# Kernel tuning notes

Hardware: AMD Instinct MI355X
Metric: run time of the kernel (lower is better)

## Reference

```python
import jax, jax.numpy as jnp
import numpy as np

N = 50000
IN_CH = 512
OUT_CH = 512
DEG = 32
E = N * DEG


def setup_inputs() -> dict:
    key = jax.random.key(0)
    kx, kwc, kwn, kb, ke = jax.random.split(key, 5)
    x = jax.random.normal(kx, (N, IN_CH), dtype=jnp.float32)
    bound = 1.0 / np.sqrt(IN_CH)
    wc = jax.random.uniform(kwc, (IN_CH, OUT_CH), minval=-bound, maxval=bound, dtype=jnp.float32)
    wn = jax.random.uniform(kwn, (IN_CH, OUT_CH), minval=-bound, maxval=bound, dtype=jnp.float32)
    bias = jax.random.uniform(kb, (OUT_CH,), minval=-bound, maxval=bound, dtype=jnp.float32)
    # Every node appears as a source exactly DEG times -> no empty-neighborhood NaNs.
    src = jnp.repeat(jnp.arange(N, dtype=jnp.int64), DEG)
    dst = jax.random.randint(ke, (E,), 0, N, dtype=jnp.int64)
    edge_index = jnp.stack([src, dst], axis=0)  # [2, E]
    return {"x": x, "wc": wc, "wn": wn, "bias": bias, "edge_index": edge_index}


def reference(x, wc, wn, bias, edge_index):
    # alpha = x @ wc ; beta = x @ wn
    alpha = x @ wc                       # [N, out]
    beta = x @ wn                        # [N, out]
    src, dst = edge_index[0], edge_index[1]
    # gamma[n] = mean_{e: src[e]==n} beta[dst[e]]
    sums = jax.ops.segment_sum(beta[dst], src, num_segments=x.shape[0])          # [N, out]
    counts = jax.ops.segment_sum(jnp.ones_like(src, dtype=beta.dtype), src,
                                 num_segments=x.shape[0])                        # [N]
    gamma = sums / counts[:, None]
    return alpha + gamma + bias
```

## Files before the change

### kernel.cpp

```cpp
#include <hip/hip_runtime.h>


#define M_ROWS 50000
#define DEG 32
#define NE (M_ROWS * DEG)

typedef short s16x8 __attribute__((ext_vector_type(8)));
typedef float f32x4 __attribute__((ext_vector_type(4)));
typedef float f32x2 __attribute__((ext_vector_type(2)));

__device__ __forceinline__ unsigned short f2bf(float f) {
  union { float f; unsigned int u; } c; c.f = f;
  unsigned int u = c.u;
  u += 0x7fffu + ((u >> 16) & 1u);
  return (unsigned short)(u >> 16);
}

__device__ __forceinline__ unsigned char f2fp8(float f) {
  int p = __builtin_amdgcn_cvt_pk_fp8_f32(f, f, 0, false);
  return (unsigned char)(p & 0xff);
}

__device__ __forceinline__ float bfhi(unsigned int u) {
  return __uint_as_float(u & 0xffff0000u);
}
__device__ __forceinline__ float bflo(unsigned int u) {
  return __uint_as_float(u << 16);
}

__device__ __forceinline__ void gl_lds16(const void* g, void* l) {
  __builtin_amdgcn_global_load_lds(
      (const __attribute__((address_space(1))) unsigned int*)g,
      (__attribute__((address_space(3))) unsigned int*)l, 16, 0, 0);
}

__global__ __launch_bounds__(256) void k_convert_x(
    const float* __restrict__ x, unsigned short* __restrict__ xb) {
  const size_t base = ((size_t)blockIdx.x * 256 + threadIdx.x) * 8;
  const float4 a = *(const float4*)(x + base);
  const float4 b = *(const float4*)(x + base + 4);
  union { unsigned short u[8]; uint4 v; } p;
  p.u[0] = f2bf(a.x); p.u[1] = f2bf(a.y); p.u[2] = f2bf(a.z); p.u[3] = f2bf(a.w);
  p.u[4] = f2bf(b.x); p.u[5] = f2bf(b.y); p.u[6] = f2bf(b.z); p.u[7] = f2bf(b.w);
  *(uint4*)(xb + base) = p.v;
}

__global__ __launch_bounds__(256) void k_convert_w(
    const float* __restrict__ wc, const float* __restrict__ wn,
    unsigned short* __restrict__ wt) {
  const int k = blockIdx.x;
  const int n4 = threadIdx.x * 4;
  const float* src = (n4 < 512) ? (wc + (size_t)k * 512 + n4)
                                : (wn + (size_t)k * 512 + (n4 - 512));
  const float4 v = *(const float4*)src;
  wt[(size_t)(n4 + 0) * 512 + k] = f2bf(v.x);
  wt[(size_t)(n4 + 1) * 512 + k] = f2bf(v.y);
  wt[(size_t)(n4 + 2) * 512 + k] = f2bf(v.z);
  wt[(size_t)(n4 + 3) * 512 + k] = f2bf(v.w);
}

__global__ __launch_bounds__(256) void k_gemm(
    const unsigned short* __restrict__ xb,
    const unsigned short* __restrict__ wt,
    const float* __restrict__ bias,
    unsigned short* __restrict__ alphab,
    unsigned char* __restrict__ betaf8) {
  __shared__ __attribute__((aligned(16))) unsigned short As[128 * 32];
  __shared__ __attribute__((aligned(16))) unsigned short Bs[128 * 32];

  const int tid = threadIdx.x;
  const int n0 = blockIdx.x * 128;
  const int m0 = blockIdx.y * 128;
  const int wv = tid >> 6;
  const int l = tid & 63;
  const int lm = l & 15;
  const int quad = l >> 4;
  const int mb = (wv >> 1) * 64;
  const int nb = (wv & 1) * 64;

  f32x4 acc[4][4];
#pragma unroll
  for (int i = 0; i < 4; ++i)
#pragma unroll
    for (int j = 0; j < 4; ++j) acc[i][j] = (f32x4)(0.0f);

  for (int kt = 0; kt < 16; ++kt) {
    const int k0 = kt * 32;
    __syncthreads();
#pragma unroll
    for (int s = 0; s < 2; ++s) {
      const int c = s * 256 + tid;
      const int row = c >> 2;
      const int seg = c & 3;
      int am = m0 + row; if (am >= M_ROWS) am = M_ROWS - 1;
      gl_lds16(xb + (size_t)am * 512 + (k0 + seg * 8),
               (char*)As + (size_t)(s * 256 + (tid & ~63)) * 16);
      gl_lds16(wt + (size_t)(n0 + row) * 512 + (k0 + seg * 8),
               (char*)Bs + (size_t)(s * 256 + (tid & ~63)) * 16);
    }
    __syncthreads();

    s16x8 af[4], bfr[4];
#pragma unroll
    for (int i = 0; i < 4; ++i)
      af[i] = *(const s16x8*)&As[(mb + 16 * i + lm) * 32 + quad * 8];
#pragma unroll
    for (int j = 0; j < 4; ++j)
      bfr[j] = *(const s16x8*)&Bs[(nb + 16 * j + lm) * 32 + quad * 8];
#pragma unroll
    for (int i = 0; i < 4; ++i)
#pragma unroll
      for (int j = 0; j < 4; ++j)
        acc[i][j] = __builtin_amdgcn_mfma_f32_16x16x32_bf16(
            af[i], bfr[j], acc[i][j], 0, 0, 0);
  }

  const bool isAlpha = (n0 < 512);
#pragma unroll
  for (int i = 0; i < 4; ++i) {
#pragma unroll
    for (int j = 0; j < 4; ++j) {
#pragma unroll
      for (int r = 0; r < 4; ++r) {
        const int m = m0 + mb + 16 * i + quad * 4 + r;
        if (m < M_ROWS) {
          const int n = n0 + nb + 16 * j + lm;
          const float v = acc[i][j][r];
          if (isAlpha) {
            alphab[(size_t)m * 512 + n] = f2bf(v + bias[n]);
          } else {
            betaf8[(size_t)m * 512 + (n - 512)] = f2fp8(v);
          }
        }
      }
    }
  }
}

__global__ __launch_bounds__(256) void k_gather(
    const int* __restrict__ dst, const uint2* __restrict__ beta8,
    const unsigned short* __restrict__ alphab, float* __restrict__ out) {
  const int node = blockIdx.x * 4 + (threadIdx.x >> 6);
  const int l = threadIdx.x & 63;
  const int idx = dst[(size_t)node * 32 + (l & 31)];
  f32x2 a01 = (f32x2)(0.0f), a23 = (f32x2)(0.0f),
        a45 = (f32x2)(0.0f), a67 = (f32x2)(0.0f);
#pragma unroll
  for (int j = 0; j < 32; ++j) {
    const int d = __builtin_amdgcn_readlane(idx, j);
    const uint2 b = beta8[(size_t)d * 64 + l];
    a01 += __builtin_amdgcn_cvt_pk_f32_fp8(b.x, false);
    a23 += __builtin_amdgcn_cvt_pk_f32_fp8(b.x, true);
    a45 += __builtin_amdgcn_cvt_pk_f32_fp8(b.y, false);
    a67 += __builtin_amdgcn_cvt_pk_f32_fp8(b.y, true);
  }
  const uint4 av = *(const uint4*)(alphab + (size_t)node * 512 + l * 8);
  const float s = 1.0f / 32.0f;
  float4 o0, o1;
  o0.x = bflo(av.x) + a01.x * s;
  o0.y = bfhi(av.x) + a01.y * s;
  o0.z = bflo(av.y) + a23.x * s;
  o0.w = bfhi(av.y) + a23.y * s;
  o1.x = bflo(av.z) + a45.x * s;
  o1.y = bfhi(av.z) + a45.y * s;
  o1.z = bflo(av.w) + a67.x * s;
  o1.w = bfhi(av.w) + a67.y * s;
  float4* o = (float4*)(out + (size_t)node * 512 + l * 8);
  o[0] = o0; o[1] = o1;
}

extern "C" void kernel_launch(void* const* d_in, const int* in_sizes, int n_in,
                              void* d_out, int out_size, void* d_ws, size_t ws_size,
                              hipStream_t stream) {
  const float* x    = (const float*)d_in[0];
  const float* wc   = (const float*)d_in[1];
  const float* wn   = (const float*)d_in[2];
  const float* bias = (const float*)d_in[3];
  const int*   ei   = (const int*)d_in[4];
  float* out = (float*)d_out;

  char* ws = (char*)d_ws;
  unsigned short* xb     = (unsigned short*)ws;
  unsigned short* wt     = (unsigned short*)(ws + 51200000);
  unsigned short* alphab = (unsigned short*)(ws + 52248576);
  unsigned char*  betaf8 = (unsigned char*)(ws + 103448576);

  k_convert_x<<<12500, 256, 0, stream>>>(x, xb);
  k_convert_w<<<512, 256, 0, stream>>>(wc, wn, wt);
  k_gemm<<<dim3(8, 391), 256, 0, stream>>>(xb, wt, bias, alphab, betaf8);
  k_gather<<<12500, 256, 0, stream>>>(ei + NE, (const uint2*)betaf8, alphab, out);
}
```

Baseline: 422.9 us.

## Widen GEMM K-tile with LDS swizzle, group tiles, and column-phase the gather

The GEMM now stages 64-wide K slices with an XOR-swizzled LDS layout to avoid bank conflicts. It precomputes load offsets, remaps blocks into groups of 8 M-tiles for better L2 reuse of activations, and hoists the bias loads. The gather is split into 8 column phases via a second grid dimension, so each phase touches only a 64-byte slice of every beta row. That keeps the randomly accessed working set small enough to stay L2-resident, with edges spread over lane groups and combined by cross-lane shuffles. The trade-off is narrower 4-byte gather loads, 8x more gather blocks, and only a quarter of the lanes doing the final stores.

```diff
diff --git a/kernel.cpp b/kernel.cpp
--- a/kernel.cpp
+++ b/kernel.cpp
@@ -65,12 +65,22 @@
     const float* __restrict__ bias,
     unsigned short* __restrict__ alphab,
     unsigned char* __restrict__ betaf8) {
-  __shared__ __attribute__((aligned(16))) unsigned short As[128 * 32];
-  __shared__ __attribute__((aligned(16))) unsigned short Bs[128 * 32];
+  __shared__ __attribute__((aligned(16))) unsigned short As[128 * 64];
+  __shared__ __attribute__((aligned(16))) unsigned short Bs[128 * 64];
 
   const int tid = threadIdx.x;
-  const int n0 = blockIdx.x * 128;
-  const int m0 = blockIdx.y * 128;
+  const int g = blockIdx.x;
+  int mt, nt;
+  if (g < 3072) {
+    const int c = g & 7, j = g >> 3;
+    nt = j & 7; mt = (j >> 3) * 8 + c;
+  } else {
+    const int r = g - 3072;
+    mt = 384 + (r >> 3); nt = r & 7;
+  }
+  const int n0 = nt * 128;
+  const int m0 = mt * 128;
+
   const int wv = tid >> 6;
   const int l = tid & 63;
   const int lm = l & 15;
@@ -78,44 +88,64 @@
   const int mb = (wv >> 1) * 64;
   const int nb = (wv & 1) * 64;
 
+  size_t aofs[4], bofs[4];
+  int ldst[4];
+#pragma unroll
+  for (int s = 0; s < 4; ++s) {
+    const int c = s * 256 + tid;
+    const int row = c >> 3;
+    const int seg = c & 7;
+    const int sg = seg ^ (row & 7);
+    int am = m0 + row; if (am >= M_ROWS) am = M_ROWS - 1;
+    aofs[s] = (size_t)am * 512 + sg * 8;
+    bofs[s] = (size_t)(n0 + row) * 512 + sg * 8;
+    ldst[s] = (s * 256 + (tid & ~63)) * 16;
+  }
+
   f32x4 acc[4][4];
 #pragma unroll
   for (int i = 0; i < 4; ++i)
 #pragma unroll
     for (int j = 0; j < 4; ++j) acc[i][j] = (f32x4)(0.0f);
 
-  for (int kt = 0; kt < 16; ++kt) {
-    const int k0 = kt * 32;
+  for (int kt = 0; kt < 8; ++kt) {
+    const int k0 = kt * 64;
     __syncthreads();
 #pragma unroll
-    for (int s = 0; s < 2; ++s) {
-      const int c = s * 256 + tid;
-      const int row = c >> 2;
-      const int seg = c & 3;
-      int am = m0 + row; if (am >= M_ROWS) am = M_ROWS - 1;
-      gl_lds16(xb + (size_t)am * 512 + (k0 + seg * 8),
-               (char*)As + (size_t)(s * 256 + (tid & ~63)) * 16);
-      gl_lds16(wt + (size_t)(n0 + row) * 512 + (k0 + seg * 8),
-               (char*)Bs + (size_t)(s * 256 + (tid & ~63)) * 16);
+    for (int s = 0; s < 4; ++s) {
+      gl_lds16(xb + aofs[s] + k0, (char*)As + ldst[s]);
+      gl_lds16(wt + bofs[s] + k0, (char*)Bs + ldst[s]);
     }
     __syncthreads();
 
-    s16x8 af[4], bfr[4];
-#pragma unroll
-    for (int i = 0; i < 4; ++i)
-      af[i] = *(const s16x8*)&As[(mb + 16 * i + lm) * 32 + quad * 8];
-#pragma unroll
-    for (int j = 0; j < 4; ++j)
-      bfr[j] = *(const s16x8*)&Bs[(nb + 16 * j + lm) * 32 + quad * 8];
-#pragma unroll
-    for (int i = 0; i < 4; ++i)
-#pragma unroll
-      for (int j = 0; j < 4; ++j)
-        acc[i][j] = __builtin_amdgcn_mfma_f32_16x16x32_bf16(
-            af[i], bfr[j], acc[i][j], 0, 0, 0);
+#pragma unroll
+    for (int h = 0; h < 2; ++h) {
+      s16x8 af[4], bfr[4];
+#pragma unroll
+      for (int i = 0; i < 4; ++i) {
+        const int R = mb + 16 * i + lm;
+        af[i] = *(const s16x8*)&As[R * 64 + (((h * 4 + quad) ^ (R & 7)) << 3)];
+      }
+#pragma unroll
+      for (int j = 0; j < 4; ++j) {
+        const int R = nb + 16 * j + lm;
+        bfr[j] = *(const s16x8*)&Bs[R * 64 + (((h * 4 + quad) ^ (R & 7)) << 3)];
+      }
+#pragma unroll
+      for (int i = 0; i < 4; ++i)
+#pragma unroll
+        for (int j = 0; j < 4; ++j)
+          acc[i][j] = __builtin_amdgcn_mfma_f32_16x16x32_bf16(
+              af[i], bfr[j], acc[i][j], 0, 0, 0);
+    }
   }
 
   const bool isAlpha = (n0 < 512);
+  float b4[4];
+#pragma unroll
+  for (int j = 0; j < 4; ++j)
+    b4[j] = isAlpha ? bias[n0 + nb + 16 * j + lm] : 0.0f;
+
 #pragma unroll
   for (int i = 0; i < 4; ++i) {
 #pragma unroll
@@ -127,7 +157,7 @@
           const int n = n0 + nb + 16 * j + lm;
           const float v = acc[i][j][r];
           if (isAlpha) {
-            alphab[(size_t)m * 512 + n] = f2bf(v + bias[n]);
+            alphab[(size_t)m * 512 + n] = f2bf(v + b4[j]);
           } else {
             betaf8[(size_t)m * 512 + (n - 512)] = f2fp8(v);
           }
@@ -138,35 +168,42 @@
 }
 
 __global__ __launch_bounds__(256) void k_gather(
-    const int* __restrict__ dst, const uint2* __restrict__ beta8,
+    const int* __restrict__ dst, const unsigned int* __restrict__ beta8,
     const unsigned short* __restrict__ alphab, float* __restrict__ out) {
+  const int phase = blockIdx.y;
   const int node = blockIdx.x * 4 + (threadIdx.x >> 6);
   const int l = threadIdx.x & 63;
+  const int grp = l >> 4;
+  const int lm = l & 15;
   const int idx = dst[(size_t)node * 32 + (l & 31)];
-  f32x2 a01 = (f32x2)(0.0f), a23 = (f32x2)(0.0f),
-        a45 = (f32x2)(0.0f), a67 = (f32x2)(0.0f);
-#pragma unroll
-  for (int j = 0; j < 32; ++j) {
-    const int d = __builtin_amdgcn_readlane(idx, j);
-    const uint2 b = beta8[(size_t)d * 64 + l];
-    a01 += __builtin_amdgcn_cvt_pk_f32_fp8(b.x, false);
-    a23 += __builtin_amdgcn_cvt_pk_f32_fp8(b.x, true);
-    a45 += __builtin_amdgcn_cvt_pk_f32_fp8(b.y, false);
-    a67 += __builtin_amdgcn_cvt_pk_f32_fp8(b.y, true);
-  }
-  const uint4 av = *(const uint4*)(alphab + (size_t)node * 512 + l * 8);
-  const float s = 1.0f / 32.0f;
-  float4 o0, o1;
-  o0.x = bflo(av.x) + a01.x * s;
-  o0.y = bfhi(av.x) + a01.y * s;
-  o0.z = bflo(av.y) + a23.x * s;
-  o0.w = bfhi(av.y) + a23.y * s;
-  o1.x = bflo(av.z) + a45.x * s;
-  o1.y = bfhi(av.z) + a45.y * s;
-  o1.z = bflo(av.w) + a67.x * s;
-  o1.w = bfhi(av.w) + a67.y * s;
-  float4* o = (float4*)(out + (size_t)node * 512 + l * 8);
-  o[0] = o0; o[1] = o1;
+
+  const unsigned int* bp = beta8 + phase * 16 + lm;
+  f32x2 s01 = (f32x2)(0.0f), s23 = (f32x2)(0.0f);
+#pragma unroll
+  for (int j = 0; j < 8; ++j) {
+    const int row = __shfl(idx, j * 4 + grp, 64);
+    const unsigned int b = bp[(size_t)row * 128];
+    s01 += __builtin_amdgcn_cvt_pk_f32_fp8(b, false);
+    s23 += __builtin_amdgcn_cvt_pk_f32_fp8(b, true);
+  }
+#pragma unroll
+  for (int off = 16; off < 64; off <<= 1) {
+    s01.x += __shfl_xor(s01.x, off, 64);
+    s01.y += __shfl_xor(s01.y, off, 64);
+    s23.x += __shfl_xor(s23.x, off, 64);
+    s23.y += __shfl_xor(s23.y, off, 64);
+  }
+  if (l < 16) {
+    const size_t o = (size_t)node * 512 + phase * 64 + lm * 4;
+    const uint2 av = *(const uint2*)(alphab + o);
+    const float s = 1.0f / 32.0f;
+    float4 v;
+    v.x = bflo(av.x) + s01.x * s;
+    v.y = bfhi(av.x) + s01.y * s;
+    v.z = bflo(av.y) + s23.x * s;
+    v.w = bfhi(av.y) + s23.y * s;
+    *(float4*)(out + o) = v;
+  }
 }
 
 extern "C" void kernel_launch(void* const* d_in, const int* in_sizes, int n_in,
@@ -187,6 +224,7 @@
 
   k_convert_x<<<12500, 256, 0, stream>>>(x, xb);
   k_convert_w<<<512, 256, 0, stream>>>(wc, wn, wt);
-  k_gemm<<<dim3(8, 391), 256, 0, stream>>>(xb, wt, bias, alphab, betaf8);
-  k_gather<<<12500, 256, 0, stream>>>(ei + NE, (const uint2*)betaf8, alphab, out);
-}
+  k_gemm<<<3128, 256, 0, stream>>>(xb, wt, bias, alphab, betaf8);
+  k_gather<<<dim3(12500, 8), 256, 0, stream>>>(ei + NE, (const unsigned int*)betaf8,
+                                               alphab, out);
+}
```

Result: no change. 420.2 us (-0.6%).
